# Optimization experiments

Measured on AMD Instinct MI355X. Metric: run time of the kernel, lower is better.

## Reference

```python
import jax, jax.numpy as jnp
import numpy as np

H, C = 4, 64          # heads, per-head out_channels (hidden_dim // heads)
D = 256               # hidden_dim
DE = 128              # edge_dim
N_ROWS, N_TOKENS, E = 20000, 100000, 300000
SCALE = 1.0 / np.sqrt(C).astype(np.float32)
EPS = 1e-5


def _lin(key, din, dout):
    k1, k2 = jax.random.split(key)
    W = jax.random.normal(k1, (din, dout), jnp.float32) * 0.05
    b = jax.random.normal(k2, (dout,), jnp.float32) * 0.05
    return W, b


def setup_inputs() -> dict:
    key = jax.random.key(0)
    ks = jax.random.split(key, 26)
    inp = {
        "row_x": jax.random.normal(ks[0], (N_ROWS, D), jnp.float32),
        "token_x": jax.random.normal(ks[1], (N_TOKENS, D), jnp.float32),
        "t2r_edge_index": jax.random.randint(ks[2], (2, E), 0, N_ROWS, jnp.int64),
        "edge_attr_t2r": jax.random.normal(ks[3], (E, DE), jnp.float32),
        "r2t_edge_index": jax.random.randint(ks[4], (2, E), 0, N_ROWS, jnp.int64),
        "edge_attr_r2t": jax.random.normal(ks[5], (E, DE), jnp.float32),
    }
    i = 6
    for p in ("t2r", "r2t"):
        for nm, din in (("q", D), ("k", D), ("v", D), ("e", DE), ("s", D)):
            W, b = _lin(ks[i], din, D); i += 1
            inp[p + "_W" + nm] = W
            inp[p + "_b" + nm] = b
    inp["row_gamma"] = jnp.ones((D,), jnp.float32)
    inp["row_beta"] = jnp.zeros((D,), jnp.float32)
    inp["token_gamma"] = jnp.ones((D,), jnp.float32)
    inp["token_beta"] = jnp.zeros((D,), jnp.float32)
    return inp


def _transformer_conv(x_src, x_dst, ei, ea, Wq, bq, Wk, bk, Wv, bv, We, be, Ws, bs):
    """PyG TransformerConv (concat=True, root_weight=True, edge_dim set, eval)."""
    N = x_dst.shape[0]
    q = (x_dst @ Wq + bq).reshape(N, H, C)       # [N_dst,H,C]
    k = (x_src @ Wk + bk).reshape(-1, H, C)      # [N_src,H,C]
    v = (x_src @ Wv + bv).reshape(-1, H, C)
    e = (ea @ We + be).reshape(-1, H, C)         # [E,H,C]
    src, dst = ei[0], ei[1]
    kj = k[src] + e                              # key_j + edge
    logits = jnp.einsum('ehc,ehc->eh', q[dst], kj) * SCALE  # [E,H]
    amax = jax.ops.segment_max(logits, dst, num_segments=N)  # [N,H]
    ex = jnp.exp(logits - amax[dst])
    denom = jax.ops.segment_sum(ex, dst, num_segments=N)
    alpha = ex / denom[dst]                      # segment softmax over dst
    msg = jax.ops.segment_sum((v[src] + e) * alpha[..., None], dst, num_segments=N)
    return msg.reshape(N, H * C) + x_dst @ Ws + bs  # concat heads + skip lin


def _ln(x, g, b):
    m = jnp.mean(x, -1, keepdims=True)
    var = jnp.mean(jnp.square(x - m), -1, keepdims=True)
    return (x - m) * jax.lax.rsqrt(var + EPS) * g + b


def reference(row_x, token_x, t2r_edge_index, edge_attr_t2r, r2t_edge_index, edge_attr_r2t,
              t2r_Wq, t2r_bq, t2r_Wk, t2r_bk, t2r_Wv, t2r_bv, t2r_We, t2r_be, t2r_Ws, t2r_bs,
              r2t_Wq, r2t_bq, r2t_Wk, r2t_bk, r2t_Wv, r2t_bv, r2t_We, r2t_be, r2t_Ws, r2t_bs,
              row_gamma, row_beta, token_gamma, token_beta):
    row_msg = _transformer_conv(token_x, row_x, t2r_edge_index, edge_attr_t2r,
                                t2r_Wq, t2r_bq, t2r_Wk, t2r_bk, t2r_Wv, t2r_bv,
                                t2r_We, t2r_be, t2r_Ws, t2r_bs)
    row_out = _ln(row_x + row_msg, row_gamma, row_beta)
    tok_msg = _transformer_conv(row_out, token_x, r2t_edge_index, edge_attr_r2t,
                                r2t_Wq, r2t_bq, r2t_Wk, r2t_bk, r2t_Wv, r2t_bv,
                                r2t_We, r2t_be, r2t_Ws, r2t_bs)
    token_out = _ln(token_x + tok_msg, token_gamma, token_beta)
    return row_out, token_out
```

## Files before the change

kernel.cpp:

```cpp
#include <hip/hip_runtime.h>
#include <cstdint>
#include <cstddef>

#define NMAX 100000
#define EMAX 300000

typedef __bf16 bf16_t;
typedef __bf16 bf16x8 __attribute__((ext_vector_type(8)));
typedef float f32x4 __attribute__((ext_vector_type(4)));
typedef unsigned int u32;

__device__ unsigned short g_mega[(size_t)NMAX * 1024];
__device__ unsigned short g_qs [(size_t)NMAX * 512];
__device__ unsigned short g_kv [(size_t)NMAX * 512];
__device__ unsigned short g_eb1[(size_t)EMAX * 256];
__device__ unsigned short g_eb2[(size_t)EMAX * 256];
__device__ unsigned short g_bfA[(size_t)NMAX * 256];
__device__ unsigned short g_bfB[(size_t)NMAX * 256];
__device__ unsigned short g_bfW[589824];
__device__ float g_bias[2560];
__device__ int   g_deg [NMAX + 1];
__device__ int   g_rp1 [NMAX + 1];
__device__ int   g_rp2 [NMAX + 1];
__device__ int   g_cur [NMAX];
__device__ int   g_ps1 [EMAX];
__device__ int   g_ps2 [EMAX];
__device__ int   g_inv1[EMAX];
__device__ int   g_inv2[EMAX];
__device__ int   g_bsum[512];

struct P4  { const float* p[4]; };
struct P10 { const float* p[10]; };

__device__ __forceinline__ unsigned short f2bf(float f) {
  unsigned u = __float_as_uint(f);
  return (unsigned short)((u + 0x7fffu + ((u >> 16) & 1u)) >> 16);
}
__device__ __forceinline__ void dec8(uint4 u, float* f) {
  f[0] = __uint_as_float(u.x << 16); f[1] = __uint_as_float(u.x & 0xffff0000u);
  f[2] = __uint_as_float(u.y << 16); f[3] = __uint_as_float(u.y & 0xffff0000u);
  f[4] = __uint_as_float(u.z << 16); f[5] = __uint_as_float(u.z & 0xffff0000u);
  f[6] = __uint_as_float(u.w << 16); f[7] = __uint_as_float(u.w & 0xffff0000u);
}

__global__ __launch_bounds__(256) void conv_bf16(const float* __restrict__ in,
                                                 unsigned short* __restrict__ out,
                                                 long long n8) {
  long long i = (long long)blockIdx.x * 256 + threadIdx.x;
  if (i >= n8) return;
  const float4* p = (const float4*)(in + i * 8);
  float4 a = p[0], b = p[1];
  ushort4 lo = make_ushort4(f2bf(a.x), f2bf(a.y), f2bf(a.z), f2bf(a.w));
  ushort4 hi = make_ushort4(f2bf(b.x), f2bf(b.y), f2bf(b.z), f2bf(b.w));
  ushort4* q = (ushort4*)(out + i * 8);
  q[0] = lo; q[1] = hi;
}

__global__ __launch_bounds__(256) void wconv4(P4 Ws, unsigned short* __restrict__ Wt,
                                              int K, int NN) {
  int i = blockIdx.x * 256 + threadIdx.x;
  if (i >= NN * K) return;
  int n = i / K, k = i - n * K;
  Wt[i] = f2bf(Ws.p[n >> 8][(size_t)k * 256 + (n & 255)]);
}

__global__ __launch_bounds__(256) void bconcat(P10 b, float* __restrict__ out) {
  int i = blockIdx.x * 256 + threadIdx.x;
  if (i < 2560) out[i] = b.p[i >> 8][i & 255];
}

#define GLL16(gp, lp) __builtin_amdgcn_global_load_lds( \
    (const __attribute__((address_space(1))) void*)(gp), \
    (__attribute__((address_space(3))) void*)(lp), 16, 0, 0)

template <int K, int NS, bool AF32>
__global__ __launch_bounds__(256) void gemm_mfma(const void* __restrict__ Av,
                                                 const unsigned short* __restrict__ Bt,
                                                 const float* __restrict__ bias,
                                                 unsigned short* __restrict__ C, int M,
                                                 const int* __restrict__ inv) {
  constexpr int NC  = NS / 128;
  constexpr int LNC = (NC == 8) ? 3 : (NC == 4) ? 2 : 1;
  const int g = blockIdx.x;
  const int r8 = g & 7;
  const int cch = (g >> 3) & (NC - 1);
  const int q8 = g >> (3 + LNC);
  const int mt = q8 * 8 + r8;
  if (mt * 128 >= M) return;
  const int bm = mt * 128, bn = cch * 128;

  __shared__ __align__(16) unsigned short As[128 * 64];
  __shared__ __align__(16) unsigned short Bs[128 * 64];
  const int tid = threadIdx.x;
  const int lane = tid & 63, wid = tid >> 6;
  const int wrow = (wid & 1) * 64, wcol = (wid >> 1) * 64;
  const int sr = lane >> 3;
  const int slot = lane & 7;

  f32x4 acc[4][4] = {};

  for (int k0 = 0; k0 < K; k0 += 64) {
    {
#pragma unroll
      for (int r = 0; r < 4; ++r) {
        int col = (wid * 4 + r) * 8 + sr;
        int kk = k0 + ((slot ^ (col & 7)) << 3);
        GLL16(Bt + (size_t)(bn + col) * K + kk, (unsigned short*)Bs + (size_t)(wid * 4 + r) * 512);
      }
    }
    if constexpr (AF32) {
      const float* Af = (const float*)Av;
#pragma unroll
      for (int r = 0; r < 4; ++r) {
        int row = (wid * 4 + r) * 8 + sr;
        int arow = bm + row; if (arow >= M) arow = M - 1;
        int kk = k0 + ((slot ^ (row & 7)) << 3);
        const float* ap = Af + (size_t)arow * K + kk;
        float4 f0 = *(const float4*)ap;
        float4 f1 = *(const float4*)(ap + 4);
        bf16x8 a;
        a[0] = (bf16_t)f0.x; a[1] = (bf16_t)f0.y; a[2] = (bf16_t)f0.z; a[3] = (bf16_t)f0.w;
        a[4] = (bf16_t)f1.x; a[5] = (bf16_t)f1.y; a[6] = (bf16_t)f1.z; a[7] = (bf16_t)f1.w;
        *(bf16x8*)((char*)As + (size_t)row * 128 + (size_t)(slot << 4)) = a;
      }
    } else {
      const unsigned short* Af = (const unsigned short*)Av;
#pragma unroll
      for (int r = 0; r < 4; ++r) {
        int row = (wid * 4 + r) * 8 + sr;
        int arow = bm + row; if (arow >= M) arow = M - 1;
        int kk = k0 + ((slot ^ (row & 7)) << 3);
        GLL16(Af + (size_t)arow * K + kk, (unsigned short*)As + (size_t)(wid * 4 + r) * 512);
      }
    }
    __syncthreads();
    const char* Ab = (const char*)As;
    const char* Bb = (const char*)Bs;
#pragma unroll
    for (int h = 0; h < 2; ++h) {
      bf16x8 af[4], bfr[4];
      int g2 = (lane >> 4) + h * 4;
#pragma unroll
      for (int fm = 0; fm < 4; ++fm) {
        int row = wrow + fm * 16 + (lane & 15);
        af[fm] = *(const bf16x8*)(Ab + row * 128 + ((g2 ^ (row & 7)) << 4));
      }
#pragma unroll
      for (int fn = 0; fn < 4; ++fn) {
        int col = wcol + fn * 16 + (lane & 15);
        bfr[fn] = *(const bf16x8*)(Bb + col * 128 + ((g2 ^ (col & 7)) << 4));
      }
#pragma unroll
      for (int fm = 0; fm < 4; ++fm)
#pragma unroll
        for (int fn = 0; fn < 4; ++fn)
          acc[fm][fn] = __builtin_amdgcn_mfma_f32_16x16x32_bf16(af[fm], bfr[fn],
                                                                acc[fm][fn], 0, 0, 0);
    }
    __syncthreads();
  }
  float bv[4];
#pragma unroll
  for (int fn = 0; fn < 4; ++fn) bv[fn] = bias[bn + wcol + fn * 16 + (lane & 15)];
#pragma unroll
  for (int fm = 0; fm < 4; ++fm) {
    int rbase = bm + wrow + fm * 16 + ((lane >> 4) << 2);
#pragma unroll
    for (int j = 0; j < 4; ++j) {
      int row = rbase + j;
      if (row < M) {
        size_t orow = inv ? (size_t)inv[row] : (size_t)row;
        size_t rb = orow * NS + bn + wcol + (lane & 15);
#pragma unroll
        for (int fn = 0; fn < 4; ++fn)
          C[rb + fn * 16] = f2bf(acc[fm][fn][j] + bv[fn]);
      }
    }
  }
}

__global__ __launch_bounds__(256) void hist_kernel(const int* __restrict__ ei,
                                                   int* __restrict__ deg, int E) {
  int i = blockIdx.x * 256 + threadIdx.x;
  if (i < E) atomicAdd(&deg[ei[E + i]], 1);
}

__global__ __launch_bounds__(256) void scan1(const int* __restrict__ deg,
                                             int* __restrict__ rowptr,
                                             int* __restrict__ bsum, int n) {
  __shared__ int ws[4];
  int i = blockIdx.x * 256 + threadIdx.x;
  int v = (i < n) ? deg[i] : 0;
  int lane = threadIdx.x & 63, wid = threadIdx.x >> 6;
  int inc = v;
#pragma unroll
  for (int o = 1; o < 64; o <<= 1) {
    int t = __shfl_up(inc, o);
    if (lane >= o) inc += t;
  }
  if (lane == 63) ws[wid] = inc;
  __syncthreads();
  int woff = 0;
  if (wid > 0) woff += ws[0];
  if (wid > 1) woff += ws[1];
  if (wid > 2) woff += ws[2];
  if (i < n) rowptr[i] = inc - v + woff;
  if (threadIdx.x == 255) bsum[blockIdx.x] = inc + woff;
}

__global__ __launch_bounds__(512) void scan2(int* __restrict__ bsum, int B) {
  __shared__ int s[512];
  int t = threadIdx.x;
  int v = (t < B) ? bsum[t] : 0;
  s[t] = v;
  __syncthreads();
  for (int o = 1; o < 512; o <<= 1) {
    int a = (t >= o) ? s[t - o] : 0;
    __syncthreads();
    s[t] += a;
    __syncthreads();
  }
  if (t < B) bsum[t] = s[t] - v;
}

__global__ __launch_bounds__(256) void scan3(int* __restrict__ rowptr,
                                             const int* __restrict__ bsum,
                                             const int* __restrict__ deg,
                                             int* __restrict__ cur, int n) {
  int i = blockIdx.x * 256 + threadIdx.x;
  if (i < n) {
    int r = rowptr[i] + bsum[blockIdx.x];
    rowptr[i] = r;
    cur[i] = r;
    if (i == n - 1) rowptr[n] = r + deg[i];
  }
}

__global__ __launch_bounds__(256) void scatter_kernel(const int* __restrict__ ei,
                                                      int* __restrict__ cur,
                                                      int* __restrict__ psrc,
                                                      int* __restrict__ inv, int E) {
  int i = blockIdx.x * 256 + threadIdx.x;
  if (i < E) {
    int s = ei[i];
    int d = ei[E + i];
    int pos = atomicAdd(&cur[d], 1);
    psrc[pos] = s;
    inv[i] = pos;
  }
}

__global__ __launch_bounds__(256) void fused_attn_ln(
    const int* __restrict__ rowptr, const int* __restrict__ psrc,
    const unsigned short* __restrict__ qs, int qs_stride,
    const unsigned short* __restrict__ kv, int kv_stride,
    const unsigned short* __restrict__ eb,
    const float* __restrict__ x,
    const float* __restrict__ gamma, const float* __restrict__ beta,
    float* __restrict__ out, unsigned short* __restrict__ out_bf, int N) {
  int node = blockIdx.x * 8 + (threadIdx.x >> 5);
  if (node >= N) return;
  int sub = threadIdx.x & 31;
  int c8 = sub << 3;
  uint4 qu = *(const uint4*)(qs + (size_t)node * qs_stride + c8);
  uint4 su = *(const uint4*)(qs + (size_t)node * qs_stride + 256 + c8);
  size_t base = (size_t)node * 256 + c8;
  float4 xv0 = *(const float4*)(x + base);
  float4 xv1 = *(const float4*)(x + base + 4);
  float q[8], s[8];
  dec8(qu, q); dec8(su, s);
  float acc[8] = {0.f, 0.f, 0.f, 0.f, 0.f, 0.f, 0.f, 0.f};
  float m = -1e30f, den = 0.f;
  int beg = rowptr[node], end = rowptr[node + 1];
  int src = (beg < end) ? psrc[beg] : 0;
  uint4 ku = *(const uint4*)(kv + (size_t)src * kv_stride + c8);
  uint4 vu = *(const uint4*)(kv + (size_t)src * kv_stride + 256 + c8);
  uint4 eu = *(const uint4*)(eb + (size_t)((beg < end) ? beg : 0) * 256 + c8);
  for (int p_ = beg; p_ < end; ++p_) {
    int pn = (p_ + 1 < end) ? (p_ + 1) : p_;
    int srcN = psrc[pn];
    uint4 kuN = *(const uint4*)(kv + (size_t)srcN * kv_stride + c8);
    uint4 vuN = *(const uint4*)(kv + (size_t)srcN * kv_stride + 256 + c8);
    uint4 euN = *(const uint4*)(eb + (size_t)pn * 256 + c8);
    float kf[8], vf[8], ef[8];
    dec8(ku, kf); dec8(vu, vf); dec8(eu, ef);
    float p = 0.f;
#pragma unroll
    for (int j = 0; j < 8; ++j) p += q[j] * (kf[j] + ef[j]);
    p += __shfl_xor(p, 1); p += __shfl_xor(p, 2); p += __shfl_xor(p, 4);
    p *= 0.125f;
    float mn = fmaxf(m, p);
    float sc = expf(m - mn);
    float w  = expf(p - mn);
    den = den * sc + w;
#pragma unroll
    for (int j = 0; j < 8; ++j) acc[j] = acc[j] * sc + w * (vf[j] + ef[j]);
    m = mn;
    ku = kuN; vu = vuN; eu = euN;
  }
  float inv = (den > 0.f) ? 1.0f / den : 0.f;
  float val[8];
  val[0] = xv0.x + s[0] + acc[0] * inv; val[1] = xv0.y + s[1] + acc[1] * inv;
  val[2] = xv0.z + s[2] + acc[2] * inv; val[3] = xv0.w + s[3] + acc[3] * inv;
  val[4] = xv1.x + s[4] + acc[4] * inv; val[5] = xv1.y + s[5] + acc[5] * inv;
  val[6] = xv1.z + s[6] + acc[6] * inv; val[7] = xv1.w + s[7] + acc[7] * inv;
  float t = 0.f;
#pragma unroll
  for (int j = 0; j < 8; ++j) t += val[j];
#pragma unroll
  for (int o = 1; o < 32; o <<= 1) t += __shfl_xor(t, o);
  float mean = t * (1.0f / 256.0f);
  float d[8], ss = 0.f;
#pragma unroll
  for (int j = 0; j < 8; ++j) { d[j] = val[j] - mean; ss += d[j] * d[j]; }
#pragma unroll
  for (int o = 1; o < 32; o <<= 1) ss += __shfl_xor(ss, o);
  float rstd = rsqrtf(ss * (1.0f / 256.0f) + 1e-5f);
  float4 g0 = *(const float4*)(gamma + c8);
  float4 g1 = *(const float4*)(gamma + c8 + 4);
  float4 b0 = *(const float4*)(beta + c8);
  float4 b1 = *(const float4*)(beta + c8 + 4);
  float o8[8];
  o8[0] = d[0] * rstd * g0.x + b0.x; o8[1] = d[1] * rstd * g0.y + b0.y;
  o8[2] = d[2] * rstd * g0.z + b0.z; o8[3] = d[3] * rstd * g0.w + b0.w;
  o8[4] = d[4] * rstd * g1.x + b1.x; o8[5] = d[5] * rstd * g1.y + b1.y;
  o8[6] = d[6] * rstd * g1.z + b1.z; o8[7] = d[7] * rstd * g1.w + b1.w;
  *(float4*)(out + base)     = make_float4(o8[0], o8[1], o8[2], o8[3]);
  *(float4*)(out + base + 4) = make_float4(o8[4], o8[5], o8[6], o8[7]);
  if (out_bf) {
    uint4 ob;
    ob.x = (u32)f2bf(o8[0]) | ((u32)f2bf(o8[1]) << 16);
    ob.y = (u32)f2bf(o8[2]) | ((u32)f2bf(o8[3]) << 16);
    ob.z = (u32)f2bf(o8[4]) | ((u32)f2bf(o8[5]) << 16);
    ob.w = (u32)f2bf(o8[6]) | ((u32)f2bf(o8[7]) << 16);
    *(uint4*)(out_bf + base) = ob;
  }
}

extern "C" void kernel_launch(void* const* d_in, const int* in_sizes, int n_in,
                              void* d_out, int out_size, void* d_ws, size_t ws_size,
                              hipStream_t stream) {
  const float* row_x   = (const float*)d_in[0];
  const float* token_x = (const float*)d_in[1];
  const int*   ei1     = (const int*)d_in[2];
  const float* ea1     = (const float*)d_in[3];
  const int*   ei2     = (const int*)d_in[4];
  const float* ea2     = (const float*)d_in[5];

  const float* W1q = (const float*)d_in[6];  const float* b1q = (const float*)d_in[7];
  const float* W1k = (const float*)d_in[8];  const float* b1k = (const float*)d_in[9];
  const float* W1v = (const float*)d_in[10]; const float* b1v = (const float*)d_in[11];
  const float* W1e = (const float*)d_in[12]; const float* b1e = (const float*)d_in[13];
  const float* W1s = (const float*)d_in[14]; const float* b1s = (const float*)d_in[15];
  const float* W2q = (const float*)d_in[16]; const float* b2q = (const float*)d_in[17];
  const float* W2k = (const float*)d_in[18]; const float* b2k = (const float*)d_in[19];
  const float* W2v = (const float*)d_in[20]; const float* b2v = (const float*)d_in[21];
  const float* W2e = (const float*)d_in[22]; const float* b2e = (const float*)d_in[23];
  const float* W2s = (const float*)d_in[24]; const float* b2s = (const float*)d_in[25];
  const float* row_gamma   = (const float*)d_in[26];
  const float* row_beta    = (const float*)d_in[27];
  const float* token_gamma = (const float*)d_in[28];
  const float* token_beta  = (const float*)d_in[29];

  const int NR = in_sizes[0] / 256;
  const int NT = in_sizes[1] / 256;
  const int E  = in_sizes[2] / 2;

  float* out_row = (float*)d_out;
  float* out_tok = (float*)d_out + (long long)NR * 256;

  void *pmega_, *pqs_, *pkv_, *peb1_, *peb2_, *pbfA_, *pbfB_, *pbfW_, *pbias_,
       *pdeg_, *prp1_, *prp2_, *pcur_, *pps1_, *pps2_, *pinv1_, *pinv2_, *pbs_;
  hipGetSymbolAddress(&pmega_, HIP_SYMBOL(g_mega));
  hipGetSymbolAddress(&pqs_,   HIP_SYMBOL(g_qs));
  hipGetSymbolAddress(&pkv_,   HIP_SYMBOL(g_kv));
  hipGetSymbolAddress(&peb1_,  HIP_SYMBOL(g_eb1));
  hipGetSymbolAddress(&peb2_,  HIP_SYMBOL(g_eb2));
  hipGetSymbolAddress(&pbfA_,  HIP_SYMBOL(g_bfA));
  hipGetSymbolAddress(&pbfB_,  HIP_SYMBOL(g_bfB));
  hipGetSymbolAddress(&pbfW_,  HIP_SYMBOL(g_bfW));
  hipGetSymbolAddress(&pbias_, HIP_SYMBOL(g_bias));
  hipGetSymbolAddress(&pdeg_,  HIP_SYMBOL(g_deg));
  hipGetSymbolAddress(&prp1_,  HIP_SYMBOL(g_rp1));
  hipGetSymbolAddress(&prp2_,  HIP_SYMBOL(g_rp2));
  hipGetSymbolAddress(&pcur_,  HIP_SYMBOL(g_cur));
  hipGetSymbolAddress(&pps1_,  HIP_SYMBOL(g_ps1));
  hipGetSymbolAddress(&pps2_,  HIP_SYMBOL(g_ps2));
  hipGetSymbolAddress(&pinv1_, HIP_SYMBOL(g_inv1));
  hipGetSymbolAddress(&pinv2_, HIP_SYMBOL(g_inv2));
  hipGetSymbolAddress(&pbs_,   HIP_SYMBOL(g_bsum));
  unsigned short* mega = (unsigned short*)pmega_;
  unsigned short* qs   = (unsigned short*)pqs_;
  unsigned short* kv   = (unsigned short*)pkv_;
  unsigned short* eb1  = (unsigned short*)peb1_;
  unsigned short* eb2  = (unsigned short*)peb2_;
  unsigned short* bfA  = (unsigned short*)pbfA_;
  unsigned short* bfB  = (unsigned short*)pbfB_;
  unsigned short* bfW  = (unsigned short*)pbfW_;
  float* gbias = (float*)pbias_;
  int*   deg   = (int*)pdeg_;
  int*   rp1   = (int*)prp1_;
  int*   rp2   = (int*)prp2_;
  int*   cur   = (int*)pcur_;
  int*   ps1   = (int*)pps1_;
  int*   ps2   = (int*)pps2_;
  int*   inv1  = (int*)pinv1_;
  int*   inv2  = (int*)pinv2_;
  int*   bsum  = (int*)pbs_;

  unsigned short* Wmega = bfW + 0;
  unsigned short* Wqs1  = bfW + 262144;
  unsigned short* Wkv2  = bfW + 393216;
  unsigned short* We1   = bfW + 524288;
  unsigned short* We2   = bfW + 557056;
  wconv4<<<1024, 256, 0, stream>>>(P4{{W1k, W1v, W2q, W2s}}, Wmega, 256, 1024);
  wconv4<<<512, 256, 0, stream>>>(P4{{W1q, W1s, nullptr, nullptr}}, Wqs1, 256, 512);
  wconv4<<<512, 256, 0, stream>>>(P4{{W2k, W2v, nullptr, nullptr}}, Wkv2, 256, 512);
  wconv4<<<128, 256, 0, stream>>>(P4{{W1e, nullptr, nullptr, nullptr}}, We1, 128, 256);
  wconv4<<<128, 256, 0, stream>>>(P4{{W2e, nullptr, nullptr, nullptr}}, We2, 128, 256);
  P10 bp{{b1k, b1v, b2q, b2s, b1q, b1s, b2k, b2v, b1e, b2e}};
  bconcat<<<10, 256, 0, stream>>>(bp, gbias);

  conv_bf16<<<(int)(((long long)NT * 32 + 255) / 256), 256, 0, stream>>>(
      token_x, bfA, (long long)NT * 32);

  const int egrid = (E + 255) / 256;

  auto csr = [&](const int* ei, int Ndst, int* rp, int* psrc, int* inv) {
    hipMemsetAsync(deg, 0, (size_t)(Ndst + 1) * sizeof(int), stream);
    hist_kernel<<<egrid, 256, 0, stream>>>(ei, deg, E);
    int B = (Ndst + 255) / 256;
    scan1<<<B, 256, 0, stream>>>(deg, rp, bsum, Ndst);
    scan2<<<1, 512, 0, stream>>>(bsum, B);
    scan3<<<B, 256, 0, stream>>>(rp, bsum, deg, cur, Ndst);
    scatter_kernel<<<egrid, 256, 0, stream>>>(ei, cur, psrc, inv, E);
  };

  csr(ei1, NR, rp1, ps1, inv1);
  csr(ei2, NT, rp2, ps2, inv2);

  auto swgrid = [](int M, int NC) {
    int nm = (M + 127) / 128;
    return (((nm + 7) / 8) * 8) * NC;
  };

  gemm_mfma<256, 1024, false><<<swgrid(NT, 8), 256, 0, stream>>>(
      bfA, Wmega, gbias + 0, mega, NT, nullptr);
  gemm_mfma<256, 512, true><<<swgrid(NR, 4), 256, 0, stream>>>(
      row_x, Wqs1, gbias + 1024, qs, NR, nullptr);
  gemm_mfma<128, 256, true><<<swgrid(E, 2), 256, 0, stream>>>(
      ea1, We1, gbias + 2048, eb1, E, inv1);
  gemm_mfma<128, 256, true><<<swgrid(E, 2), 256, 0, stream>>>(
      ea2, We2, gbias + 2304, eb2, E, inv2);

  fused_attn_ln<<<(NR + 7) / 8, 256, 0, stream>>>(rp1, ps1,
                                                  qs, 512, mega, 1024, eb1,
                                                  row_x, row_gamma, row_beta,
                                                  out_row, bfB, NR);

  gemm_mfma<256, 512, false><<<swgrid(NR, 4), 256, 0, stream>>>(
      bfB, Wkv2, gbias + 1536, kv, NR, nullptr);
  fused_attn_ln<<<(NT + 7) / 8, 256, 0, stream>>>(rp2, ps2,
                                                  mega + 512, 1024, kv, 512, eb2,
                                                  token_x, token_gamma, token_beta,
                                                  out_tok, nullptr, NT);
}
```

Measured before the change: 634.8 us.

## Merge CSR builds for both graphs, drop softmax max tracking, read bf16 residual

Builds the histogram and scatter passes for both edge sets in single combined launches over a doubled degree/cursor buffer. This cuts kernel launches and memsets. The attention loop drops the online-softmax running max and accumulates exp(logit) directly, which saves one exp and the rescaling per edge but can overflow for large logits. The token-side residual is now read from the existing bf16 copy of token_x instead of fp32, which halves that load at some loss of precision.

```diff
diff --git a/kernel.cpp b/kernel.cpp
--- a/kernel.cpp
+++ b/kernel.cpp
@@ -19,10 +19,10 @@
 __device__ unsigned short g_bfB[(size_t)NMAX * 256];
 __device__ unsigned short g_bfW[589824];
 __device__ float g_bias[2560];
-__device__ int   g_deg [NMAX + 1];
+__device__ int   g_degc[2 * (NMAX + 1)];
 __device__ int   g_rp1 [NMAX + 1];
 __device__ int   g_rp2 [NMAX + 1];
-__device__ int   g_cur [NMAX];
+__device__ int   g_curc[2 * NMAX];
 __device__ int   g_ps1 [EMAX];
 __device__ int   g_ps2 [EMAX];
 __device__ int   g_inv1[EMAX];
@@ -179,10 +179,12 @@
   }
 }
 
-__global__ __launch_bounds__(256) void hist_kernel(const int* __restrict__ ei,
-                                                   int* __restrict__ deg, int E) {
-  int i = blockIdx.x * 256 + threadIdx.x;
-  if (i < E) atomicAdd(&deg[ei[E + i]], 1);
+__global__ __launch_bounds__(256) void hist2_kernel(const int* __restrict__ ei1,
+                                                    const int* __restrict__ ei2,
+                                                    int* __restrict__ deg, int E) {
+  int i = blockIdx.x * 256 + threadIdx.x;
+  if (i < E) atomicAdd(&deg[ei1[E + i]], 1);
+  else if (i < 2 * E) atomicAdd(&deg[(NMAX + 1) + ei2[E + (i - E)]], 1);
 }
 
 __global__ __launch_bounds__(256) void scan1(const int* __restrict__ deg,
@@ -236,17 +238,25 @@
   }
 }
 
-__global__ __launch_bounds__(256) void scatter_kernel(const int* __restrict__ ei,
-                                                      int* __restrict__ cur,
-                                                      int* __restrict__ psrc,
-                                                      int* __restrict__ inv, int E) {
+__global__ __launch_bounds__(256) void scatter2_kernel(const int* __restrict__ ei1,
+                                                       const int* __restrict__ ei2,
+                                                       int* __restrict__ cur,
+                                                       int* __restrict__ ps1,
+                                                       int* __restrict__ ps2,
+                                                       int* __restrict__ inv1,
+                                                       int* __restrict__ inv2, int E) {
   int i = blockIdx.x * 256 + threadIdx.x;
   if (i < E) {
-    int s = ei[i];
-    int d = ei[E + i];
+    int s = ei1[i], d = ei1[E + i];
     int pos = atomicAdd(&cur[d], 1);
-    psrc[pos] = s;
-    inv[i] = pos;
+    ps1[pos] = s;
+    inv1[i] = pos;
+  } else if (i < 2 * E) {
+    int j = i - E;
+    int s = ei2[j], d = ei2[E + j];
+    int pos = atomicAdd(&cur[NMAX + d], 1);
+    ps2[pos] = s;
+    inv2[j] = pos;
   }
 }
 
@@ -255,7 +265,7 @@
     const unsigned short* __restrict__ qs, int qs_stride,
     const unsigned short* __restrict__ kv, int kv_stride,
     const unsigned short* __restrict__ eb,
-    const float* __restrict__ x,
+    const float* __restrict__ xf, const unsigned short* __restrict__ xb,
     const float* __restrict__ gamma, const float* __restrict__ beta,
     float* __restrict__ out, unsigned short* __restrict__ out_bf, int N) {
   int node = blockIdx.x * 8 + (threadIdx.x >> 5);
@@ -265,12 +275,20 @@
   uint4 qu = *(const uint4*)(qs + (size_t)node * qs_stride + c8);
   uint4 su = *(const uint4*)(qs + (size_t)node * qs_stride + 256 + c8);
   size_t base = (size_t)node * 256 + c8;
-  float4 xv0 = *(const float4*)(x + base);
-  float4 xv1 = *(const float4*)(x + base + 4);
+  float xv[8];
+  if (xb) {
+    uint4 xu = *(const uint4*)(xb + base);
+    dec8(xu, xv);
+  } else {
+    float4 x0 = *(const float4*)(xf + base);
+    float4 x1 = *(const float4*)(xf + base + 4);
+    xv[0] = x0.x; xv[1] = x0.y; xv[2] = x0.z; xv[3] = x0.w;
+    xv[4] = x1.x; xv[5] = x1.y; xv[6] = x1.z; xv[7] = x1.w;
+  }
   float q[8], s[8];
   dec8(qu, q); dec8(su, s);
   float acc[8] = {0.f, 0.f, 0.f, 0.f, 0.f, 0.f, 0.f, 0.f};
-  float m = -1e30f, den = 0.f;
+  float den = 0.f;
   int beg = rowptr[node], end = rowptr[node + 1];
   int src = (beg < end) ? psrc[beg] : 0;
   uint4 ku = *(const uint4*)(kv + (size_t)src * kv_stride + c8);
@@ -288,22 +306,16 @@
 #pragma unroll
     for (int j = 0; j < 8; ++j) p += q[j] * (kf[j] + ef[j]);
     p += __shfl_xor(p, 1); p += __shfl_xor(p, 2); p += __shfl_xor(p, 4);
-    p *= 0.125f;
-    float mn = fmaxf(m, p);
-    float sc = expf(m - mn);
-    float w  = expf(p - mn);
-    den = den * sc + w;
-#pragma unroll
-    for (int j = 0; j < 8; ++j) acc[j] = acc[j] * sc + w * (vf[j] + ef[j]);
-    m = mn;
+    float w = expf(p * 0.125f);
+    den += w;
+#pragma unroll
+    for (int j = 0; j < 8; ++j) acc[j] += w * (vf[j] + ef[j]);
     ku = kuN; vu = vuN; eu = euN;
   }
   float inv = (den > 0.f) ? 1.0f / den : 0.f;
   float val[8];
-  val[0] = xv0.x + s[0] + acc[0] * inv; val[1] = xv0.y + s[1] + acc[1] * inv;
-  val[2] = xv0.z + s[2] + acc[2] * inv; val[3] = xv0.w + s[3] + acc[3] * inv;
-  val[4] = xv1.x + s[4] + acc[4] * inv; val[5] = xv1.y + s[5] + acc[5] * inv;
-  val[6] = xv1.z + s[6] + acc[6] * inv; val[7] = xv1.w + s[7] + acc[7] * inv;
+#pragma unroll
+  for (int j = 0; j < 8; ++j) val[j] = xv[j] + s[j] + acc[j] * inv;
   float t = 0.f;
 #pragma unroll
   for (int j = 0; j < 8; ++j) t += val[j];
@@ -380,10 +392,10 @@
   hipGetSymbolAddress(&pbfB_,  HIP_SYMBOL(g_bfB));
   hipGetSymbolAddress(&pbfW_,  HIP_SYMBOL(g_bfW));
   hipGetSymbolAddress(&pbias_, HIP_SYMBOL(g_bias));
-  hipGetSymbolAddress(&pdeg_,  HIP_SYMBOL(g_deg));
+  hipGetSymbolAddress(&pdeg_,  HIP_SYMBOL(g_degc));
   hipGetSymbolAddress(&prp1_,  HIP_SYMBOL(g_rp1));
   hipGetSymbolAddress(&prp2_,  HIP_SYMBOL(g_rp2));
-  hipGetSymbolAddress(&pcur_,  HIP_SYMBOL(g_cur));
+  hipGetSymbolAddress(&pcur_,  HIP_SYMBOL(g_curc));
   hipGetSymbolAddress(&pps1_,  HIP_SYMBOL(g_ps1));
   hipGetSymbolAddress(&pps2_,  HIP_SYMBOL(g_ps2));
   hipGetSymbolAddress(&pinv1_, HIP_SYMBOL(g_inv1));
@@ -424,20 +436,21 @@
   conv_bf16<<<(int)(((long long)NT * 32 + 255) / 256), 256, 0, stream>>>(
       token_x, bfA, (long long)NT * 32);
 
-  const int egrid = (E + 255) / 256;
-
-  auto csr = [&](const int* ei, int Ndst, int* rp, int* psrc, int* inv) {
-    hipMemsetAsync(deg, 0, (size_t)(Ndst + 1) * sizeof(int), stream);
-    hist_kernel<<<egrid, 256, 0, stream>>>(ei, deg, E);
-    int B = (Ndst + 255) / 256;
-    scan1<<<B, 256, 0, stream>>>(deg, rp, bsum, Ndst);
-    scan2<<<1, 512, 0, stream>>>(bsum, B);
-    scan3<<<B, 256, 0, stream>>>(rp, bsum, deg, cur, Ndst);
-    scatter_kernel<<<egrid, 256, 0, stream>>>(ei, cur, psrc, inv, E);
-  };
-
-  csr(ei1, NR, rp1, ps1, inv1);
-  csr(ei2, NT, rp2, ps2, inv2);
+  const int e2grid = (2 * E + 255) / 256;
+
+  hipMemsetAsync(deg, 0, (size_t)(2 * (NMAX + 1)) * sizeof(int), stream);
+  hist2_kernel<<<e2grid, 256, 0, stream>>>(ei1, ei2, deg, E);
+  {
+    int B1 = (NR + 255) / 256;
+    scan1<<<B1, 256, 0, stream>>>(deg, rp1, bsum, NR);
+    scan2<<<1, 512, 0, stream>>>(bsum, B1);
+    scan3<<<B1, 256, 0, stream>>>(rp1, bsum, deg, cur, NR);
+    int B2 = (NT + 255) / 256;
+    scan1<<<B2, 256, 0, stream>>>(deg + NMAX + 1, rp2, bsum, NT);
+    scan2<<<1, 512, 0, stream>>>(bsum, B2);
+    scan3<<<B2, 256, 0, stream>>>(rp2, bsum, deg + NMAX + 1, cur + NMAX, NT);
+  }
+  scatter2_kernel<<<e2grid, 256, 0, stream>>>(ei1, ei2, cur, ps1, ps2, inv1, inv2, E);
 
   auto swgrid = [](int M, int NC) {
     int nm = (M + 127) / 128;
@@ -455,13 +468,15 @@
 
   fused_attn_ln<<<(NR + 7) / 8, 256, 0, stream>>>(rp1, ps1,
                                                   qs, 512, mega, 1024, eb1,
-                                                  row_x, row_gamma, row_beta,
+                                                  row_x, nullptr,
+                                                  row_gamma, row_beta,
                                                   out_row, bfB, NR);
 
   gemm_mfma<256, 512, false><<<swgrid(NR, 4), 256, 0, stream>>>(
       bfB, Wkv2, gbias + 1536, kv, NR, nullptr);
   fused_attn_ln<<<(NT + 7) / 8, 256, 0, stream>>>(rp2, ps2,
                                                   mega + 512, 1024, kv, 512, eb2,
-                                                  token_x, token_gamma, token_beta,
+                                                  nullptr, bfA,
+                                                  token_gamma, token_beta,
                                                   out_tok, nullptr, NT);
 }
```

After: 605.4 us. -4.6%, faster.
